# Kernel optimization log

Measured on AMD Instinct MI355X. Metric: run time of the kernel, lower is better.

The kernel has to match this reference:

```python
import jax, jax.numpy as jnp
import numpy as np

B, IN, H = 8192, 1024, 1024


def setup_inputs() -> dict:
    key = jax.random.key(0)
    ks = jax.random.split(key, 12)
    s_in = 1.0 / np.sqrt(IN + H)  # torch Linear default init scale
    inp = {
        "x": jax.random.normal(ks[0], (B, IN), jnp.float32),
        "h_prev": jax.random.normal(ks[1], (B, H), jnp.float32),
        "c_prev": jax.random.normal(ks[2], (B, H), jnp.float32),
        "embed": jax.random.normal(ks[3], (B, H), jnp.float32),
    }
    for i, g in enumerate(("forget", "input", "update", "out")):
        inp[f"W_{g}"] = jax.random.uniform(ks[4 + 2 * i], (IN + H, H), jnp.float32, -s_in, s_in)
        inp[f"b_{g}"] = jax.random.uniform(ks[5 + 2 * i], (H,), jnp.float32, -s_in, s_in)
    return inp


def reference(x, h_prev, c_prev, embed,
              W_forget, b_forget, W_input, b_input,
              W_update, b_update, W_out, b_out):
    # cat_input: [B, IN+H]; embed is accepted but unused (matches source forward)
    cat_input = jnp.concatenate((x.reshape(x.shape[0], -1), h_prev), axis=1)
    # Fuse the 4 gate GEMMs into one [B, IN+H] x [IN+H, 4H] matmul (same math)
    W = jnp.concatenate((W_forget, W_input, W_update, W_out), axis=1)  # [IN+H, 4H]
    b = jnp.concatenate((b_forget, b_input, b_update, b_out))          # [4H]
    gates = cat_input @ W + b                                          # [B, 4H]
    f_t, i_t, g_t, o_t = jnp.split(gates, 4, axis=1)
    f_t = jax.nn.sigmoid(f_t)
    i_t = jax.nn.sigmoid(i_t)
    c_opt = jnp.tanh(g_t)
    c_t = c_prev * f_t + i_t * c_opt
    o_t = jax.nn.sigmoid(o_t)
    h_t = o_t * jnp.tanh(c_t)
    return (h_t, c_t)
```

## Files before the change

### kernel.cpp

```cpp
#include <hip/hip_runtime.h>
#include <hip/hip_bf16.h>


typedef __attribute__((ext_vector_type(8))) short short8;
typedef __attribute__((ext_vector_type(4))) float f32x4;

#define GLOBAL_AS __attribute__((address_space(1)))
#define LDS_AS    __attribute__((address_space(3)))

__device__ __forceinline__ void load_lds16(const void* g, void* l) {
  __builtin_amdgcn_global_load_lds((const GLOBAL_AS unsigned int*)g,
                                   (LDS_AS unsigned int*)l, 16, 0, 0);
}

__device__ __forceinline__ unsigned short f2bf(float f) {
  unsigned int u = __float_as_uint(f);
  return (unsigned short)((u + 0x7FFFu + ((u >> 16) & 1u)) >> 16);
}
__device__ __forceinline__ float sigf(float x) { return 1.0f / (1.0f + __expf(-x)); }
__device__ __forceinline__ float tanh_fast(float x) {
  return 1.0f - 2.0f / (__expf(2.0f * x) + 1.0f);
}

__global__ void pack_kernel(const float* __restrict__ x,
                            const float* __restrict__ h,
                            const float* __restrict__ W0,
                            const float* __restrict__ W1,
                            const float* __restrict__ W2,
                            const float* __restrict__ W3,
                            unsigned short* __restrict__ Apk,
                            unsigned short* __restrict__ Wp) {
  int blk = blockIdx.x;
  if (blk < 8192) {
    int t = blk * 256 + threadIdx.x;
    int row = t >> 8;
    int c   = t & 255;
    int k   = c << 3;
    const float* src = (k < 1024) ? (x + (size_t)row * 1024 + k)
                                  : (h + (size_t)row * 1024 + (k - 1024));
    float4 f0 = ((const float4*)src)[0];
    float4 f1 = ((const float4*)src)[1];
    union { unsigned short us[8]; uint4 v; } u;
    u.us[0] = f2bf(f0.x); u.us[1] = f2bf(f0.y);
    u.us[2] = f2bf(f0.z); u.us[3] = f2bf(f0.w);
    u.us[4] = f2bf(f1.x); u.us[5] = f2bf(f1.y);
    u.us[6] = f2bf(f1.z); u.us[7] = f2bf(f1.w);
    *(uint4*)(Apk + (size_t)row * 2048 + c * 8) = u.v;
  } else {
    int b  = blk - 8192;
    int c  = b & 255;
    int nb = (b >> 8) & 3;
    int g  = b >> 10;
    const float* Wg = (g == 0) ? W0 : (g == 1) ? W1 : (g == 2) ? W2 : W3;
    int np = nb * 256 + threadIdx.x;
    int kbase = c << 3;
    union { unsigned short us[8]; uint4 v; } u;
#pragma unroll
    for (int j = 0; j < 8; ++j)
      u.us[j] = f2bf(Wg[(size_t)(kbase + j) * 1024 + np]);
    int n = (g << 10) + np;
    *(uint4*)(Wp + (size_t)n * 2048 + c * 8) = u.v;
  }
}

#define MFMA16(va, vb, vc) __builtin_amdgcn_mfma_f32_16x16x32_bf16(va, vb, vc, 0, 0, 0)

#define PHASE(J, Q, KTP, PSLOT, WAITN)                                         \
  {                                                                            \
    const int slotUS = (J) * 8192;                                             \
    short8 av[4];                                                              \
    _Pragma("unroll")                                                          \
    for (int mm = 0; mm < 4; ++mm)                                             \
      av[mm] = *(const short8*)&LDSu[slotUS + aRdBase + ((Q) * 4 + mm) * 512]; \
    if ((Q) == 0) {                                                            \
      _Pragma("unroll")                                                        \
      for (int gg = 0; gg < 4; ++gg)                                           \
        bv[gg] = *(const short8*)&LDSu[32768 + slotUS + bRdBase + gg * 512];   \
    }                                                                          \
    int ktp = (KTP); ktp = (ktp > 31) ? 31 : ktp;                              \
    const int srcOfs = ktp * 64 + ((PSLOT) & 1) * 32;                          \
    const int pbase = (PSLOT) * 8192;                                          \
    if ((Q) == 0) {                                                            \
      load_lds16(aSrc0 + srcOfs, &LDSu[pbase + wv * 512]);                     \
      load_lds16(aSrc1 + srcOfs, &LDSu[pbase + 4096 + wv * 512]);              \
    } else {                                                                   \
      load_lds16(bSrc0 + srcOfs, &LDSu[32768 + pbase + wv * 512]);             \
      load_lds16(bSrc1 + srcOfs, &LDSu[32768 + pbase + 4096 + wv * 512]);      \
    }                                                                          \
    __builtin_amdgcn_s_barrier();                                              \
    asm volatile("s_waitcnt lgkmcnt(0)");                                      \
    __builtin_amdgcn_sched_barrier(0);                                         \
    __builtin_amdgcn_s_setprio(1);                                             \
    _Pragma("unroll")                                                          \
    for (int mm = 0; mm < 4; ++mm) {                                           \
      _Pragma("unroll")                                                        \
      for (int gg = 0; gg < 4; ++gg)                                           \
        acc[(Q) * 4 + mm][gg] = MFMA16(av[mm], bv[gg], acc[(Q) * 4 + mm][gg]); \
    }                                                                          \
    __builtin_amdgcn_s_setprio(0);                                             \
    if ((WAITN) == 8) asm volatile("s_waitcnt vmcnt(8)");                      \
    if ((WAITN) == 4) asm volatile("s_waitcnt vmcnt(4)");                      \
    __builtin_amdgcn_s_barrier();                                              \
  }

__global__ __launch_bounds__(512, 2) void lstm_gemm_kernel(
    const unsigned short* __restrict__ Apk,
    const unsigned short* __restrict__ Wp,
    const float* __restrict__ c_prev,
    const float* __restrict__ bF, const float* __restrict__ bI,
    const float* __restrict__ bU, const float* __restrict__ bO,
    float* __restrict__ outH, float* __restrict__ outC) {
  extern __shared__ unsigned short LDSu[];

  const int tid = threadIdx.x;
  const int l   = tid & 63;
  const int wv  = tid >> 6;
  const int wr  = wv >> 2;
  const int wc  = wv & 3;

  int bid = blockIdx.x;
  int wg  = ((bid & 7) << 6) | (bid >> 3);
  const int mblk = wg >> 4;
  const int nblk = wg & 15;
  const int brow = mblk << 8;

  const int rl  = l & 15;
  const int cg  = l >> 4;
  const int sc  = cg ^ ((rl >> 1) & 3);
  const int aRdBase = (wr * 128 + rl) * 32 + sc * 8;
  const int bRdBase = (wc * 64 + rl) * 32 + sc * 8;

  const int srow = wv * 16 + (l >> 2);
  const int csw  = ((l & 3) ^ ((l >> 3) & 3)) * 8;
  const unsigned short* aSrc0 = Apk + (size_t)(brow + srow) * 2048 + csw;
  const unsigned short* aSrc1 = aSrc0 + (size_t)128 * 2048;
  int p0 = nblk * 256 + srow;
  int n0 = (((p0 >> 4) & 3) << 10) | ((p0 >> 6) << 4) | (p0 & 15);
  int p1 = p0 + 128;
  int n1 = (((p1 >> 4) & 3) << 10) | ((p1 >> 6) << 4) | (p1 & 15);
  const unsigned short* bSrc0 = Wp + (size_t)n0 * 2048 + csw;
  const unsigned short* bSrc1 = Wp + (size_t)n1 * 2048 + csw;

  f32x4 acc[8][4];
#pragma unroll
  for (int m = 0; m < 8; ++m)
#pragma unroll
    for (int g = 0; g < 4; ++g) acc[m][g] = (f32x4)0.0f;

  load_lds16(aSrc0 + 0,  &LDSu[0 + wv * 512]);
  load_lds16(aSrc1 + 0,  &LDSu[4096 + wv * 512]);
  load_lds16(bSrc0 + 0,  &LDSu[32768 + wv * 512]);
  load_lds16(bSrc1 + 0,  &LDSu[32768 + 4096 + wv * 512]);
  load_lds16(aSrc0 + 32, &LDSu[8192 + wv * 512]);
  load_lds16(aSrc1 + 32, &LDSu[8192 + 4096 + wv * 512]);
  load_lds16(bSrc0 + 32, &LDSu[32768 + 8192 + wv * 512]);
  load_lds16(bSrc1 + 32, &LDSu[32768 + 8192 + 4096 + wv * 512]);
  load_lds16(aSrc0 + 64, &LDSu[16384 + wv * 512]);
  load_lds16(aSrc1 + 64, &LDSu[16384 + 4096 + wv * 512]);
  load_lds16(bSrc0 + 64, &LDSu[32768 + 16384 + wv * 512]);
  load_lds16(bSrc1 + 64, &LDSu[32768 + 16384 + 4096 + wv * 512]);
  asm volatile("s_waitcnt vmcnt(4)");
  __builtin_amdgcn_s_barrier();

#pragma unroll 1
  for (int it = 0; it < 16; ++it) {
    const int k2 = it << 1;
    short8 bv[4];
    PHASE(0, 0, k2 + 1, 3, -1)
    PHASE(0, 1, k2 + 1, 3, -1)
    PHASE(1, 0, k2 + 2, 0, -1)
    PHASE(1, 1, k2 + 2, 0, 8)
    PHASE(2, 0, k2 + 2, 1, -1)
    PHASE(2, 1, k2 + 2, 1, 8)
    PHASE(3, 0, k2 + 3, 2, -1)
    PHASE(3, 1, k2 + 3, 2, 4)
  }

  const int colh = nblk * 64 + wc * 16 + rl;
  const float biasF = bF[colh], biasI = bI[colh];
  const float biasU = bU[colh], biasO = bO[colh];
  const int row0 = brow + wr * 128 + ((l >> 4) << 2);
#pragma unroll
  for (int m = 0; m < 8; ++m) {
#pragma unroll
    for (int r = 0; r < 4; ++r) {
      int row = row0 + m * 16 + r;
      size_t idx = (size_t)row * 1024 + colh;
      float f  = sigf(acc[m][0][r] + biasF);
      float i_ = sigf(acc[m][1][r] + biasI);
      float g_ = tanh_fast(acc[m][2][r] + biasU);
      float o_ = sigf(acc[m][3][r] + biasO);
      float cp = c_prev[idx];
      float cn = cp * f + i_ * g_;
      outH[idx] = o_ * tanh_fast(cn);
      outC[idx] = cn;
    }
  }
}

extern "C" void kernel_launch(void* const* d_in, const int* in_sizes, int n_in,
                              void* d_out, int out_size, void* d_ws, size_t ws_size,
                              hipStream_t stream) {
  const float* x      = (const float*)d_in[0];
  const float* h_prev = (const float*)d_in[1];
  const float* c_prev = (const float*)d_in[2];
  const float* Wf = (const float*)d_in[4];
  const float* bf = (const float*)d_in[5];
  const float* Wi = (const float*)d_in[6];
  const float* bi = (const float*)d_in[7];
  const float* Wu = (const float*)d_in[8];
  const float* bu = (const float*)d_in[9];
  const float* Wo = (const float*)d_in[10];
  const float* bo = (const float*)d_in[11];

  unsigned short* Apk = (unsigned short*)d_ws;
  unsigned short* Wp  = (unsigned short*)((char*)d_ws + (size_t)8192 * 2048 * 2);

  pack_kernel<<<12288, 256, 0, stream>>>(x, h_prev, Wf, Wi, Wu, Wo, Apk, Wp);

  hipFuncSetAttribute((const void*)lstm_gemm_kernel,
                      hipFuncAttributeMaxDynamicSharedMemorySize, 131072);

  float* outH = (float*)d_out;
  float* outC = outH + (size_t)8192 * 1024;
  lstm_gemm_kernel<<<512, 512, 131072, stream>>>(Apk, Wp, c_prev,
                                                 bf, bi, bu, bo, outH, outC);
}
```

Measured before the change: 180.0 us.

## Software-pipeline LDS fragment reads one phase ahead of MFMA compute

Restructures the K-loop so LDS reads for the next phase go into a second register set while MFMAs consume the current one, using a 4-slot ring with a 64-step schedule. This removes the lgkmcnt(0) wait and sched_barrier that serialised each phase's LDS reads ahead of its MFMAs. It also changes the vmcnt waits to a uniform vmcnt(6) with a deeper prefetch. The cost is more VGPRs for the double-buffered fragments, which may pressure the 512x2 launch bounds, plus a more intricate ring indexing that has to stay correct with the barriers.

```diff
diff --git a/kernel.cpp b/kernel.cpp
--- a/kernel.cpp
+++ b/kernel.cpp
@@ -65,41 +65,39 @@
 
 #define MFMA16(va, vb, vc) __builtin_amdgcn_mfma_f32_16x16x32_bf16(va, vb, vc, 0, 0, 0)
 
-#define PHASE(J, Q, KTP, PSLOT, WAITN)                                         \
+#define PH(ARd, rdRing, mQ, DOB, BRd, ACm, BCm, QOFF, stSlot, stIsA, DOVM)     \
   {                                                                            \
-    const int slotUS = (J) * 8192;                                             \
-    short8 av[4];                                                              \
+    const int rr_ = (rdRing);                                                  \
     _Pragma("unroll")                                                          \
     for (int mm = 0; mm < 4; ++mm)                                             \
-      av[mm] = *(const short8*)&LDSu[slotUS + aRdBase + ((Q) * 4 + mm) * 512]; \
-    if ((Q) == 0) {                                                            \
+      ARd[mm] = *(const short8*)&LDSu[rr_ * 8192 + aRdBase + ((mQ) * 4 + mm) * 512]; \
+    if (DOB) {                                                                 \
       _Pragma("unroll")                                                        \
       for (int gg = 0; gg < 4; ++gg)                                           \
-        bv[gg] = *(const short8*)&LDSu[32768 + slotUS + bRdBase + gg * 512];   \
+        BRd[gg] = *(const short8*)&LDSu[32768 + rr_ * 8192 + bRdBase + gg * 512]; \
     }                                                                          \
-    int ktp = (KTP); ktp = (ktp > 31) ? 31 : ktp;                              \
-    const int srcOfs = ktp * 64 + ((PSLOT) & 1) * 32;                          \
-    const int pbase = (PSLOT) * 8192;                                          \
-    if ((Q) == 0) {                                                            \
-      load_lds16(aSrc0 + srcOfs, &LDSu[pbase + wv * 512]);                     \
-      load_lds16(aSrc1 + srcOfs, &LDSu[pbase + 4096 + wv * 512]);              \
-    } else {                                                                   \
-      load_lds16(bSrc0 + srcOfs, &LDSu[32768 + pbase + wv * 512]);             \
-      load_lds16(bSrc1 + srcOfs, &LDSu[32768 + pbase + 4096 + wv * 512]);      \
+    {                                                                          \
+      int ss_ = (stSlot); ss_ = ss_ > 63 ? 63 : ss_;                           \
+      const int so_ = ss_ * 32;                                                \
+      const int pb_ = ((stSlot) & 3) * 8192;                                   \
+      if (stIsA) {                                                             \
+        load_lds16(aSrc0 + so_, &LDSu[pb_ + wv * 512]);                        \
+        load_lds16(aSrc1 + so_, &LDSu[pb_ + 4096 + wv * 512]);                 \
+      } else {                                                                 \
+        load_lds16(bSrc0 + so_, &LDSu[32768 + pb_ + wv * 512]);                \
+        load_lds16(bSrc1 + so_, &LDSu[32768 + pb_ + 4096 + wv * 512]);         \
+      }                                                                        \
     }                                                                          \
     __builtin_amdgcn_s_barrier();                                              \
-    asm volatile("s_waitcnt lgkmcnt(0)");                                      \
-    __builtin_amdgcn_sched_barrier(0);                                         \
     __builtin_amdgcn_s_setprio(1);                                             \
     _Pragma("unroll")                                                          \
     for (int mm = 0; mm < 4; ++mm) {                                           \
       _Pragma("unroll")                                                        \
       for (int gg = 0; gg < 4; ++gg)                                           \
-        acc[(Q) * 4 + mm][gg] = MFMA16(av[mm], bv[gg], acc[(Q) * 4 + mm][gg]); \
+        acc[(QOFF) + mm][gg] = MFMA16(ACm[mm], BCm[gg], acc[(QOFF) + mm][gg]); \
     }                                                                          \
     __builtin_amdgcn_s_setprio(0);                                             \
-    if ((WAITN) == 8) asm volatile("s_waitcnt vmcnt(8)");                      \
-    if ((WAITN) == 4) asm volatile("s_waitcnt vmcnt(4)");                      \
+    if (DOVM) asm volatile("s_waitcnt vmcnt(6)");                              \
     __builtin_amdgcn_s_barrier();                                              \
   }
 
@@ -159,21 +157,28 @@
   load_lds16(aSrc1 + 64, &LDSu[16384 + 4096 + wv * 512]);
   load_lds16(bSrc0 + 64, &LDSu[32768 + 16384 + wv * 512]);
   load_lds16(bSrc1 + 64, &LDSu[32768 + 16384 + 4096 + wv * 512]);
-  asm volatile("s_waitcnt vmcnt(4)");
+  asm volatile("s_waitcnt vmcnt(8)");
   __builtin_amdgcn_s_barrier();
 
+  short8 a0[4], a1[4], b0[4], b1[4];
+#pragma unroll
+  for (int mm = 0; mm < 4; ++mm)
+    a0[mm] = *(const short8*)&LDSu[aRdBase + mm * 512];
+#pragma unroll
+  for (int gg = 0; gg < 4; ++gg)
+    b0[gg] = *(const short8*)&LDSu[32768 + bRdBase + gg * 512];
+
 #pragma unroll 1
-  for (int it = 0; it < 16; ++it) {
-    const int k2 = it << 1;
-    short8 bv[4];
-    PHASE(0, 0, k2 + 1, 3, -1)
-    PHASE(0, 1, k2 + 1, 3, -1)
-    PHASE(1, 0, k2 + 2, 0, -1)
-    PHASE(1, 1, k2 + 2, 0, 8)
-    PHASE(2, 0, k2 + 2, 1, -1)
-    PHASE(2, 1, k2 + 2, 1, 8)
-    PHASE(3, 0, k2 + 3, 2, -1)
-    PHASE(3, 1, k2 + 3, 2, 4)
+  for (int u = 0; u < 32; ++u) {
+    const int ra = (u & 1) << 1;
+    const int rb = ra | 1;
+    const int rc = 2 - ra;
+    const int s3 = 2 * u + 3;
+    const int s4 = 2 * u + 4;
+    PH(a1, ra, 1, 0, b1, a0, b0, 0, s3, 1, 1)
+    PH(a0, rb, 0, 1, b1, a1, b0, 4, s3, 0, 0)
+    PH(a1, rb, 1, 0, b0, a0, b1, 0, s4, 1, 1)
+    PH(a0, rc, 0, 1, b0, a1, b1, 4, s4, 0, 0)
   }
 
   const int colh = nblk * 64 + wc * 16 + rl;
```

Result: no change. 183.5 us (+2.0%).
